# Performance work log

Hardware: AMD Instinct MI355X
Metric: run time of the kernel (lower is better)

The kernel has to match this reference:

```python
import jax, jax.numpy as jnp
import numpy as np

N = 50000          # num_entities
R = 16             # num_relations
D = 128            # embedding_dim
B = 4              # num_blocks
d = D // B         # block size (32)
E = 800000         # num edges


def setup_inputs() -> dict:
    key = jax.random.key(0)
    ks = jax.random.split(key, 9)
    s = 1.0 / np.sqrt(D)
    return {
        "edge_index": jax.random.randint(ks[0], (2, E), 0, N),
        "edge_type": jax.random.randint(ks[1], (E,), 0, R),
        "node_emb": jax.random.normal(ks[2], (N, D), jnp.float32) * s,
        "W1": jax.random.normal(ks[3], (R, B, d, d), jnp.float32) * s,
        "root1": jax.random.normal(ks[4], (D, D), jnp.float32) * s,
        "bias1": jax.random.normal(ks[5], (D,), jnp.float32) * 0.01,
        "W2": jax.random.normal(ks[6], (R, B, d, d), jnp.float32) * s,
        "root2": jax.random.normal(ks[7], (D, D), jnp.float32) * s,
        "bias2": jax.random.normal(ks[8], (D,), jnp.float32) * 0.01,
    }


def _rgcn_conv(x, src, dst, et, W, root, bias):
    # x: [N, D]; W: [R, B, d, d] block-diagonal per-relation weights.
    n = x.shape[0]
    # Transform every node under every relation (cheaper than gathering
    # per-edge weight blocks): [R, N, B, d] -> [R, N, D]
    allR = jnp.einsum('nbi,rbio->rnbo', x.reshape(n, B, d), W).reshape(R, n, D)
    msg = allR[et, src]                                   # [E, D] gather
    # Per-relation mean normalization 1/c_{i,r} (PyG RGCNConv aggr='mean'
    # applied per relation): count edges per (dst, relation) pair.
    seg = dst * R + et
    cnt = jax.ops.segment_sum(jnp.ones_like(et, x.dtype), seg, num_segments=n * R)
    norm = 1.0 / jnp.maximum(cnt[seg], 1.0)               # [E]
    agg = jax.ops.segment_sum(msg * norm[:, None], dst, num_segments=n)
    return agg + x @ root + bias


def reference(edge_index, edge_type, node_emb, W1, root1, bias1, W2, root2, bias2):
    src, dst = edge_index[0], edge_index[1]
    h = _rgcn_conv(node_emb, src, dst, edge_type, W1, root1, bias1)
    h = jax.nn.relu(h)  # dropout is identity in eval mode
    return _rgcn_conv(h, src, dst, edge_type, W2, root2, bias2)
```

## Files before the change

### kernel.cpp

```cpp
#include <hip/hip_runtime.h>
#include <hip/hip_bf16.h>

#define N_NODES 50000
#define N_REL   16
#define DIM     128
#define NBLK    4
#define BS      32
#define N_EDGES 800000
#define NSEG    (N_NODES * N_REL)
#define SCAN_BLK 1024
#define N_SCAN_BLKS ((NSEG + SCAN_BLK - 1) / SCAN_BLK)
#define NWT     (N_NODES / 16)

typedef __attribute__((ext_vector_type(8))) short s8v;
typedef __attribute__((ext_vector_type(8))) unsigned short u8v;
typedef __attribute__((ext_vector_type(4))) float f4v;

__device__ __forceinline__ float bf2f(unsigned short u) {
    return __uint_as_float(((unsigned int)u) << 16);
}
__device__ __forceinline__ unsigned short f2bfbits(float f) {
    unsigned int u = __float_as_uint(f);
    return (unsigned short)((u + 0x7fffu + ((u >> 16) & 1u)) >> 16);
}

__global__ __launch_bounds__(256) void count_kernel(const int* __restrict__ src,
                                                    const int* __restrict__ dst,
                                                    const int* __restrict__ et,
                                                    int* __restrict__ cnt,
                                                    int* __restrict__ used, int E) {
    int e = blockIdx.x * 256 + threadIdx.x;
    if (e < E) {
        int r = et[e];
        atomicAdd(&cnt[dst[e] * N_REL + r], 1);
        used[r * N_NODES + src[e]] = 1;
    }
}

__global__ __launch_bounds__(256) void scan1j_kernel(const int* __restrict__ cnt,
                                                     const int* __restrict__ used,
                                                     int* __restrict__ off,
                                                     int* __restrict__ cmap,
                                                     int2* __restrict__ bsum, int M) {
    const int t = threadIdx.x;
    const int base = blockIdx.x * SCAN_BLK + t * 4;
    int c[4], u[4];
#pragma unroll
    for (int i = 0; i < 4; ++i) {
        int idx = base + i;
        c[i] = (idx < M) ? cnt[idx] : 0;
        u[i] = (idx < M) ? used[idx] : 0;
    }
    int cs = c[0] + c[1] + c[2] + c[3];
    int us = u[0] + u[1] + u[2] + u[3];
    const int lane = t & 63, wid = t >> 6;
    int cinc = cs, uinc = us;
    for (int d = 1; d < 64; d <<= 1) {
        int a = __shfl_up(cinc, d, 64);
        int b = __shfl_up(uinc, d, 64);
        if (lane >= d) { cinc += a; uinc += b; }
    }
    __shared__ int cw[5], uw[5];
    if (lane == 63) { cw[wid] = cinc; uw[wid] = uinc; }
    __syncthreads();
    if (t == 0) {
        int a = 0, b = 0;
        for (int w = 0; w < 4; ++w) {
            int x = cw[w]; cw[w] = a; a += x;
            int y = uw[w]; uw[w] = b; b += y;
        }
        cw[4] = a; uw[4] = b;
    }
    __syncthreads();
    int cex = cinc - cs + cw[wid];
    int uex = uinc - us + uw[wid];
#pragma unroll
    for (int i = 0; i < 4; ++i) {
        int idx = base + i;
        if (idx < M) { off[idx] = cex; cmap[idx] = uex; }
        cex += c[i]; uex += u[i];
    }
    if (t == 0) bsum[blockIdx.x] = make_int2(cw[4], uw[4]);
}

__global__ __launch_bounds__(1024) void scan2j_kernel(int2* __restrict__ bsum, int nb) {
    const int t = threadIdx.x;
    int2 s = (t < nb) ? bsum[t] : make_int2(0, 0);
    const int lane = t & 63, wid = t >> 6;
    int ci = s.x, ui = s.y;
    for (int d = 1; d < 64; d <<= 1) {
        int a = __shfl_up(ci, d, 64);
        int b = __shfl_up(ui, d, 64);
        if (lane >= d) { ci += a; ui += b; }
    }
    __shared__ int cw[16], uw[16];
    if (lane == 63) { cw[wid] = ci; uw[wid] = ui; }
    __syncthreads();
    if (t == 0) {
        int a = 0, b = 0;
        for (int w = 0; w < 16; ++w) {
            int x = cw[w]; cw[w] = a; a += x;
            int y = uw[w]; uw[w] = b; b += y;
        }
    }
    __syncthreads();
    if (t < nb) bsum[t] = make_int2(ci - s.x + cw[wid], ui - s.y + uw[wid]);
}

__global__ __launch_bounds__(256) void scatter_fast_kernel(const int* __restrict__ src,
                                                           const int* __restrict__ dst,
                                                           const int* __restrict__ et,
                                                           int* __restrict__ off,
                                                           const int* __restrict__ cnt,
                                                           const int* __restrict__ cmap,
                                                           const int2* __restrict__ bsum,
                                                           int2* __restrict__ evec, int E) {
    int e = blockIdx.x * 256 + threadIdx.x;
    if (e < E) {
        int r = et[e];
        int seg = dst[e] * N_REL + r;
        int pos = atomicAdd(&off[seg], 1) + bsum[seg >> 10].x;
        float inv = 1.0f / (float)cnt[seg];
        int grow = r * N_NODES + src[e];
        int g = cmap[grow] + bsum[grow >> 10].y;
        evec[pos] = make_int2(g, __float_as_int(inv));
    }
}

__global__ __launch_bounds__(256) void scan1_kernel(const int* __restrict__ in,
                                                    int* __restrict__ out,
                                                    int* __restrict__ bsum, int M) {
    const int t = threadIdx.x;
    const int base = blockIdx.x * SCAN_BLK + t * 4;
    int v0 = (base + 0 < M) ? in[base + 0] : 0;
    int v1 = (base + 1 < M) ? in[base + 1] : 0;
    int v2 = (base + 2 < M) ? in[base + 2] : 0;
    int v3 = (base + 3 < M) ? in[base + 3] : 0;
    const int s = v0 + v1 + v2 + v3;
    const int lane = t & 63, wid = t >> 6;
    int inc = s;
    for (int d = 1; d < 64; d <<= 1) {
        int u = __shfl_up(inc, d, 64);
        if (lane >= d) inc += u;
    }
    __shared__ int wsum[5];
    if (lane == 63) wsum[wid] = inc;
    __syncthreads();
    if (t == 0) {
        int a = 0;
        for (int w = 0; w < 4; ++w) { int u = wsum[w]; wsum[w] = a; a += u; }
        wsum[4] = a;
    }
    __syncthreads();
    const int ex = inc - s + wsum[wid];
    if (base + 0 < M) out[base + 0] = ex;
    if (base + 1 < M) out[base + 1] = ex + v0;
    if (base + 2 < M) out[base + 2] = ex + v0 + v1;
    if (base + 3 < M) out[base + 3] = ex + v0 + v1 + v2;
    if (t == 0) bsum[blockIdx.x] = wsum[4];
}

__global__ __launch_bounds__(1024) void scan2_kernel(int* __restrict__ bsum, int nb) {
    const int t = threadIdx.x;
    int s = (t < nb) ? bsum[t] : 0;
    const int lane = t & 63, wid = t >> 6;
    int inc = s;
    for (int d = 1; d < 64; d <<= 1) {
        int u = __shfl_up(inc, d, 64);
        if (lane >= d) inc += u;
    }
    __shared__ int wsum[16];
    if (lane == 63) wsum[wid] = inc;
    __syncthreads();
    if (t == 0) {
        int a = 0;
        for (int w = 0; w < 16; ++w) { int u = wsum[w]; wsum[w] = a; a += u; }
    }
    __syncthreads();
    const int ex = inc - s + wsum[wid];
    if (t < nb) bsum[t] = ex;
}

__global__ __launch_bounds__(256) void scan3_kernel(int* __restrict__ out,
                                                    const int* __restrict__ bsum, int M) {
    int i = blockIdx.x * 256 + threadIdx.x;
    if (i < M) out[i] += bsum[i / SCAN_BLK];
}

__global__ __launch_bounds__(256) void scatter_old_kernel(const int* __restrict__ src,
                                                          const int* __restrict__ dst,
                                                          const int* __restrict__ et,
                                                          int* __restrict__ off,
                                                          int* __restrict__ srcs, int E) {
    int e = blockIdx.x * 256 + threadIdx.x;
    if (e < E) {
        int seg = dst[e] * N_REL + et[e];
        int pos = atomicAdd(&off[seg], 1);
        srcs[pos] = src[e];
    }
}

__global__ __launch_bounds__(256) void prep_kernel(const float* __restrict__ W1,
                                                   const float* __restrict__ W2,
                                                   const float* __restrict__ r1,
                                                   const float* __restrict__ r2,
                                                   ushort* __restrict__ WB1,
                                                   ushort* __restrict__ WB2,
                                                   ushort* __restrict__ RB1,
                                                   ushort* __restrict__ RB2) {
    int t = blockIdx.x * 256 + threadIdx.x;
    if (t < 262144) {
        const float* W = (t < 131072) ? W1 : W2;
        ushort* WB     = (t < 131072) ? WB1 : WB2;
        int idx = t & 131071;
        int i  = idx & 7;
        int lm = (idx >> 3) & 15;
        int kg = (idx >> 7) & 3;
        int mt = (idx >> 9) & 1;
        int b  = (idx >> 10) & 3;
        int r  = idx >> 12;
        WB[idx] = f2bfbits(W[((size_t)(r * 4 + b) * 32 + kg * 8 + i) * 32 + mt * 16 + lm]);
    } else if (t < 294912) {
        int u = t - 262144;
        const float* R = (u < 16384) ? r1 : r2;
        ushort* RB     = (u < 16384) ? RB1 : RB2;
        int idx = u & 16383;
        int i  = idx & 7;
        int lm = (idx >> 3) & 15;
        int kg = (idx >> 7) & 3;
        int kc = (idx >> 9) & 3;
        int mt = (idx >> 11) & 7;
        RB[idx] = f2bfbits(R[(size_t)(kc * 32 + kg * 8 + i) * DIM + mt * 16 + lm]);
    }
}

template<bool IN_BF16, bool OUT_BF16, bool RELU>
__global__ __launch_bounds__(256) void fused_kernel(const void* __restrict__ xin,
                                                    const ushort* __restrict__ WB,
                                                    const ushort* __restrict__ RB,
                                                    const float* __restrict__ bias,
                                                    const int* __restrict__ used,
                                                    const int* __restrict__ cmap,
                                                    const int2* __restrict__ bsum,
                                                    char* __restrict__ tab,
                                                    float* __restrict__ scl,
                                                    void* __restrict__ outv) {
    const int wv = threadIdx.x >> 6;
    const int l  = threadIdx.x & 63;
    const int wt = blockIdx.x * 4 + wv;
    if (wt >= NWT) return;
    const int rbase = blockIdx.y * 8;
    const int lm = l & 15;
    const int kg = l >> 4;
    const int node = wt * 16 + lm;

    s8v bfr[4];
#pragma unroll
    for (int b = 0; b < 4; ++b) {
        if (IN_BF16) {
            const ushort* xp = (const ushort*)xin + (size_t)node * DIM + b * BS + kg * 8;
            u8v u = *(const u8v*)xp;
#pragma unroll
            for (int i = 0; i < 8; ++i) {
                unsigned short us = u[i];
                if (RELU) us = (us & 0x8000u) ? (unsigned short)0 : us;
                bfr[b][i] = (short)us;
            }
        } else {
            const float* xp = (const float*)xin + (size_t)node * DIM + b * BS + kg * 8;
#pragma unroll
            for (int i = 0; i < 8; ++i) {
                float v = xp[i];
                if (RELU) v = fmaxf(v, 0.f);
                bfr[b][i] = (short)f2bfbits(v);
            }
        }
    }

#pragma unroll 2
    for (int ri = 0; ri < 8; ++ri) {
        const int rr = rbase + ri;
        const int grow = rr * N_NODES + node;
        const int flag = used[grow];
        const int cid  = cmap[grow] + bsum[grow >> 10].y;
        f4v acc[4][2];
#pragma unroll
        for (int b = 0; b < 4; ++b) {
#pragma unroll
            for (int mt = 0; mt < 2; ++mt) {
                s8v afrag = *(const s8v*)&WB[((((rr * 4 + b) * 2 + mt) * 4 + kg) * 16 + lm) * 8];
                f4v z = {0.f, 0.f, 0.f, 0.f};
                acc[b][mt] = __builtin_amdgcn_mfma_f32_16x16x32_bf16(afrag, bfr[b], z, 0, 0, 0);
            }
        }
        float t8[8];
#pragma unroll
        for (int b = 0; b < 4; ++b)
#pragma unroll
            for (int mt = 0; mt < 2; ++mt)
                t8[b * 2 + mt] = fmaxf(fmaxf(fabsf(acc[b][mt][0]), fabsf(acc[b][mt][1])),
                                       fmaxf(fabsf(acc[b][mt][2]), fabsf(acc[b][mt][3])));
        float m = fmaxf(fmaxf(fmaxf(t8[0], t8[1]), fmaxf(t8[2], t8[3])),
                        fmaxf(fmaxf(t8[4], t8[5]), fmaxf(t8[6], t8[7])));
        m = fmaxf(m, __shfl_xor(m, 16, 64));
        m = fmaxf(m, __shfl_xor(m, 32, 64));
        m = fmaxf(m, 1e-30f);

        if (flag) {
            const float qs = 127.0f / m;
            unsigned int d[8];
#pragma unroll
            for (int b = 0; b < 4; ++b) {
#pragma unroll
                for (int mt = 0; mt < 2; ++mt) {
                    int q0 = __float2int_rn(acc[b][mt][0] * qs);
                    int q1 = __float2int_rn(acc[b][mt][1] * qs);
                    int q2 = __float2int_rn(acc[b][mt][2] * qs);
                    int q3 = __float2int_rn(acc[b][mt][3] * qs);
                    unsigned int t01 = __builtin_amdgcn_perm((unsigned)q1, (unsigned)q0, 0x00000400u);
                    unsigned int t23 = __builtin_amdgcn_perm((unsigned)q3, (unsigned)q2, 0x00000400u);
                    d[b * 2 + mt] = __builtin_amdgcn_perm(t23, t01, 0x05040100u);
                }
            }
            char* gp = tab + (size_t)cid * 128 + kg * 32;
            *(uint4*)gp        = make_uint4(d[0], d[1], d[2], d[3]);
            *(uint4*)(gp + 16) = make_uint4(d[4], d[5], d[6], d[7]);
            if (kg == 0) scl[cid] = m * (1.0f / 127.0f);
        }
    }

    if (blockIdx.y == 0) {
#pragma unroll 2
        for (int mt = 0; mt < 8; ++mt) {
            const int col0 = mt * 16 + kg * 4;
            f4v acc = *(const f4v*)&bias[col0];
#pragma unroll
            for (int kc = 0; kc < 4; ++kc) {
                s8v afrag = *(const s8v*)&RB[(((mt * 4 + kc) * 4 + kg) * 16 + lm) * 8];
                acc = __builtin_amdgcn_mfma_f32_16x16x32_bf16(afrag, bfr[kc], acc, 0, 0, 0);
            }
            if (OUT_BF16) {
                unsigned int p0 = (unsigned int)f2bfbits(acc[0]) |
                                  ((unsigned int)f2bfbits(acc[1]) << 16);
                unsigned int p1 = (unsigned int)f2bfbits(acc[2]) |
                                  ((unsigned int)f2bfbits(acc[3]) << 16);
                *(uint2*)((ushort*)outv + (size_t)node * DIM + col0) = make_uint2(p0, p1);
            } else {
                *(f4v*)((float*)outv + (size_t)node * DIM + col0) = acc;
            }
        }
    }
}

template<bool OUT_BF16>
__global__ __launch_bounds__(256) void agg8_kernel(const int2* __restrict__ evec,
                                                   const int* __restrict__ off,
                                                   const int2* __restrict__ bsum,
                                                   const char* __restrict__ tab,
                                                   const float* __restrict__ scl,
                                                   void* __restrict__ outv) {
    const int hw = threadIdx.x >> 5;
    const int o  = threadIdx.x & 31;
    const int v  = blockIdx.x * 8 + hw;

    const int ei = v * N_REL + N_REL - 1;
    const int end = off[ei] + bsum[ei >> 10].x;
    int start = 0;
    if (v > 0) {
        const int si = v * N_REL - 1;
        start = off[si] + bsum[si >> 10].x;
    }

    const int p = o >> 4;
    const int w = o & 15;

    float acc[8];
#pragma unroll
    for (int j = 0; j < 8; ++j) acc[j] = 0.f;

#pragma unroll 2
    for (int base = start; base < end; base += 4) {
        const int k0 = base + p;
        const int k1 = base + 2 + p;
        const int2 e0 = evec[min(k0, end - 1)];
        const int2 e1 = evec[min(k1, end - 1)];
        const int g0 = e0.x, g1 = e1.x;
        const float i0 = (k0 < end) ? __int_as_float(e0.y) : 0.f;
        const float i1 = (k1 < end) ? __int_as_float(e1.y) : 0.f;
        const uint2 q0 = *(const uint2*)(tab + (size_t)g0 * 128 + w * 8);
        const uint2 q1 = *(const uint2*)(tab + (size_t)g1 * 128 + w * 8);
        const float s0 = scl[g0] * i0;
        const float s1 = scl[g1] * i1;
#pragma unroll
        for (int j = 0; j < 4; ++j) {
            acc[j]     = fmaf((float)(int)(signed char)(q0.x >> (8 * j)), s0, acc[j]);
            acc[4 + j] = fmaf((float)(int)(signed char)(q0.y >> (8 * j)), s0, acc[4 + j]);
        }
#pragma unroll
        for (int j = 0; j < 4; ++j) {
            acc[j]     = fmaf((float)(int)(signed char)(q1.x >> (8 * j)), s1, acc[j]);
            acc[4 + j] = fmaf((float)(int)(signed char)(q1.y >> (8 * j)), s1, acc[4 + j]);
        }
    }
#pragma unroll
    for (int j = 0; j < 8; ++j)
        acc[j] += __shfl_xor(acc[j], 16, 32);

    if (o < 16) {
        const int base0 = (o & 3) * 32 + (o >> 2) * 4;
        if (OUT_BF16) {
            ushort* hp = (ushort*)outv + (size_t)v * DIM + base0;
            ushort4 a0 = *(ushort4*)hp;
            ushort4 a1 = *(ushort4*)(hp + 16);
            a0.x = f2bfbits(bf2f(a0.x) + acc[0]);
            a0.y = f2bfbits(bf2f(a0.y) + acc[1]);
            a0.z = f2bfbits(bf2f(a0.z) + acc[2]);
            a0.w = f2bfbits(bf2f(a0.w) + acc[3]);
            a1.x = f2bfbits(bf2f(a1.x) + acc[4]);
            a1.y = f2bfbits(bf2f(a1.y) + acc[5]);
            a1.z = f2bfbits(bf2f(a1.z) + acc[6]);
            a1.w = f2bfbits(bf2f(a1.w) + acc[7]);
            *(ushort4*)hp        = a0;
            *(ushort4*)(hp + 16) = a1;
        } else {
            float* op = (float*)outv + (size_t)v * DIM + base0;
            float4 r0 = *(float4*)op;
            float4 r1 = *(float4*)(op + 16);
            r0.x += acc[0]; r0.y += acc[1]; r0.z += acc[2]; r0.w += acc[3];
            r1.x += acc[4]; r1.y += acc[5]; r1.z += acc[6]; r1.w += acc[7];
            *(float4*)op        = r0;
            *(float4*)(op + 16) = r1;
        }
    }
}

template<bool RELU>
__global__ __launch_bounds__(256) void dense_old_kernel(const float* __restrict__ x,
                                                        const float* __restrict__ root,
                                                        const float* __restrict__ bias,
                                                        float* __restrict__ out) {
    const int wv = threadIdx.x >> 6;
    const int l  = threadIdx.x & 63;
    const int wt = blockIdx.x * 4 + wv;
    if (wt >= NWT) return;
    const int nbase = wt * 16;
    const int lm = l & 15;
    const int kg = l >> 4;
    const int node = nbase + lm;

    s8v bfr[4];
#pragma unroll
    for (int kc = 0; kc < 4; ++kc) {
        const float* xp = &x[(size_t)node * DIM + kc * BS + kg * 8];
#pragma unroll
        for (int i = 0; i < 8; ++i) {
            float v = xp[i];
            if (RELU) v = fmaxf(v, 0.f);
            bfr[kc][i] = (short)f2bfbits(v);
        }
    }
#pragma unroll 2
    for (int mt = 0; mt < 8; ++mt) {
        const int col0 = mt * 16 + kg * 4;
        f4v acc = *(const f4v*)&bias[col0];
#pragma unroll
        for (int kc = 0; kc < 4; ++kc) {
            const float* rp = &root[(size_t)(kc * BS + kg * 8) * DIM + mt * 16 + lm];
            s8v afrag;
#pragma unroll
            for (int i = 0; i < 8; ++i)
                afrag[i] = (short)f2bfbits(rp[i * DIM]);
            acc = __builtin_amdgcn_mfma_f32_16x16x32_bf16(afrag, bfr[kc], acc, 0, 0, 0);
        }
        *(f4v*)&out[(size_t)node * DIM + col0] = acc;
    }
}

template<bool RELU>
__global__ __launch_bounds__(256) void agg_fallback_kernel(const int* __restrict__ srcs,
                                                           const int* __restrict__ off,
                                                           const int* __restrict__ cnt,
                                                           const float* __restrict__ x,
                                                           const float* __restrict__ W,
                                                           float* __restrict__ out) {
    __shared__ float Wsh[N_REL * BS * BS];
    const int bblk = blockIdx.y;
    for (int idx = threadIdx.x * 4; idx < N_REL * BS * BS; idx += 1024) {
        int r = idx >> 10, rest = idx & 1023;
        *(float4*)&Wsh[idx] = *(const float4*)&W[(r * NBLK + bblk) * 1024 + rest];
    }
    __syncthreads();
    const int hw = threadIdx.x >> 5;
    const int o  = threadIdx.x & 31;
    const int v  = blockIdx.x * 8 + hw;
    int endv = 0, cv = 0;
    if (o < N_REL) { endv = off[v * N_REL + o]; cv = cnt[v * N_REL + o]; }
    float acc = out[v * DIM + bblk * BS + o];
    for (int r = 0; r < N_REL; ++r) {
        const int c = __shfl(cv, r, 32);
        if (c == 0) continue;
        const int end = __shfl(endv, r, 32);
        float xs = 0.f;
        for (int k = end - c; k < end; ++k) {
            const int s = srcs[k];
            float xv = x[s * DIM + bblk * BS + o];
            if (RELU) xv = fmaxf(xv, 0.f);
            xs += xv;
        }
        xs *= (1.0f / (float)c);
        const float* wr = &Wsh[r * (BS * BS)];
#pragma unroll
        for (int i = 0; i < BS; i += 2) {
            float xi0 = __shfl(xs, i, 32);
            float xi1 = __shfl(xs, i + 1, 32);
            acc = fmaf(xi0, wr[i * BS + o], acc);
            acc = fmaf(xi1, wr[(i + 1) * BS + o], acc);
        }
    }
    out[v * DIM + bblk * BS + o] = acc;
}

extern "C" void kernel_launch(void* const* d_in, const int* in_sizes, int n_in,
                              void* d_out, int out_size, void* d_ws, size_t ws_size,
                              hipStream_t stream) {
    const int*   edge_index = (const int*)d_in[0];
    const int*   src   = edge_index;
    const int*   dstv  = edge_index + N_EDGES;
    const int*   et    = (const int*)d_in[1];
    const float* x0    = (const float*)d_in[2];
    const float* W1    = (const float*)d_in[3];
    const float* root1 = (const float*)d_in[4];
    const float* bias1 = (const float*)d_in[5];
    const float* W2    = (const float*)d_in[6];
    const float* root2 = (const float*)d_in[7];
    const float* bias2 = (const float*)d_in[8];
    float* out = (float*)d_out;

    char* ws = (char*)d_ws;
    ushort* h    = (ushort*)ws;
    int*    cnt  = (int*)   (ws + 12800000);
    int*    used = (int*)   (ws + 16000000);
    int*    off  = (int*)   (ws + 19200000);
    int*    cmap = (int*)   (ws + 22400000);
    int2*   evec = (int2*)  (ws + 25600000);
    int2*   bsum = (int2*)  (ws + 32000000);
    ushort* WB1  = (ushort*)(ws + 32008192);
    ushort* WB2  = (ushort*)(ws + 32270336);
    ushort* RB1  = (ushort*)(ws + 32532480);
    ushort* RB2  = (ushort*)(ws + 32565248);
    float*  scl  = (float*) (ws + 32598016);
    char*   tab  =          (ws + 35798016);
    const size_t FAST_NEED = 138198016ull;

    const int egrid = (N_EDGES + 255) / 256;
    const int tgrid = (NWT + 3) / 4;

    if (ws_size >= FAST_NEED) {
        prep_kernel<<<1152, 256, 0, stream>>>(W1, W2, root1, root2, WB1, WB2, RB1, RB2);
        hipMemsetAsync(cnt, 0, 2 * (size_t)NSEG * sizeof(int), stream);
        count_kernel<<<egrid, 256, 0, stream>>>(src, dstv, et, cnt, used, N_EDGES);
        scan1j_kernel<<<N_SCAN_BLKS, 256, 0, stream>>>(cnt, used, off, cmap, bsum, NSEG);
        scan2j_kernel<<<1, 1024, 0, stream>>>(bsum, N_SCAN_BLKS);
        scatter_fast_kernel<<<egrid, 256, 0, stream>>>(src, dstv, et, off, cnt, cmap,
                                                       bsum, evec, N_EDGES);

        dim3 fgrid(tgrid, 2);
        const int ngrid = N_NODES / 8;

        fused_kernel<false, true, false><<<fgrid, 256, 0, stream>>>(
            x0, WB1, RB1, bias1, used, cmap, bsum, tab, scl, h);
        agg8_kernel<true><<<ngrid, 256, 0, stream>>>(evec, off, bsum, tab, scl, h);

        fused_kernel<true, false, true><<<fgrid, 256, 0, stream>>>(
            h, WB2, RB2, bias2, used, cmap, bsum, tab, scl, out);
        agg8_kernel<false><<<ngrid, 256, 0, stream>>>(evec, off, bsum, tab, scl, out);
    } else {
        float* hf    = (float*)d_ws;
        int*   cntf  = (int*)((char*)d_ws + 25600000);
        int*   offf  = (int*)((char*)d_ws + 28800000);
        int*   srcsf = (int*)((char*)d_ws + 32000000);
        int*   bsumf = (int*)((char*)d_ws + 35200000);
        int*   usedD = offf;

        hipMemsetAsync(cntf, 0, (size_t)NSEG * sizeof(int), stream);
        count_kernel<<<egrid, 256, 0, stream>>>(src, dstv, et, cntf, usedD, N_EDGES);
        scan1_kernel<<<N_SCAN_BLKS, 256, 0, stream>>>(cntf, offf, bsumf, NSEG);
        scan2_kernel<<<1, 1024, 0, stream>>>(bsumf, N_SCAN_BLKS);
        scan3_kernel<<<(NSEG + 255) / 256, 256, 0, stream>>>(offf, bsumf, NSEG);
        scatter_old_kernel<<<egrid, 256, 0, stream>>>(src, dstv, et, offf, srcsf, N_EDGES);

        dim3 fgrid2(N_NODES / 8, NBLK);
        dense_old_kernel<false><<<tgrid, 256, 0, stream>>>(x0, root1, bias1, hf);
        agg_fallback_kernel<false><<<fgrid2, 256, 0, stream>>>(srcsf, offf, cntf, x0, W1, hf);
        dense_old_kernel<true><<<tgrid, 256, 0, stream>>>(hf, root2, bias2, out);
        agg_fallback_kernel<true><<<fgrid2, 256, 0, stream>>>(srcsf, offf, cntf, hf, W2, out);
    }
}
```

Before: 244.6 us.

## Fuse edge scatter into first transform kernel, zero counters in prep, split root work

The per-edge CSR scatter now runs as extra blocks of the first fused transform launch, so edge placement overlaps with the relation transforms and one launch is removed. The counter memset is folded into the prep kernel as a grid-stride zero loop. The dense root/bias epilogue is split across the two relation halves instead of being done only by the y=0 half. Int8 quantisation uses a magic-number FMA in place of float-to-int conversions. The fallback count kernel no longer writes into the offset buffer. Risks are heavier kernels and scatter blocks competing for resources with the transform blocks.

```diff
diff --git a/kernel.cpp b/kernel.cpp
--- a/kernel.cpp
+++ b/kernel.cpp
@@ -11,6 +11,8 @@
 #define SCAN_BLK 1024
 #define N_SCAN_BLKS ((NSEG + SCAN_BLK - 1) / SCAN_BLK)
 #define NWT     (N_NODES / 16)
+#define NWTB    ((NWT + 3) / 4)
+#define SCATB   ((N_EDGES + 511) / 512)
 
 typedef __attribute__((ext_vector_type(8))) short s8v;
 typedef __attribute__((ext_vector_type(8))) unsigned short u8v;
@@ -22,182 +24,6 @@
 __device__ __forceinline__ unsigned short f2bfbits(float f) {
     unsigned int u = __float_as_uint(f);
     return (unsigned short)((u + 0x7fffu + ((u >> 16) & 1u)) >> 16);
-}
-
-__global__ __launch_bounds__(256) void count_kernel(const int* __restrict__ src,
-                                                    const int* __restrict__ dst,
-                                                    const int* __restrict__ et,
-                                                    int* __restrict__ cnt,
-                                                    int* __restrict__ used, int E) {
-    int e = blockIdx.x * 256 + threadIdx.x;
-    if (e < E) {
-        int r = et[e];
-        atomicAdd(&cnt[dst[e] * N_REL + r], 1);
-        used[r * N_NODES + src[e]] = 1;
-    }
-}
-
-__global__ __launch_bounds__(256) void scan1j_kernel(const int* __restrict__ cnt,
-                                                     const int* __restrict__ used,
-                                                     int* __restrict__ off,
-                                                     int* __restrict__ cmap,
-                                                     int2* __restrict__ bsum, int M) {
-    const int t = threadIdx.x;
-    const int base = blockIdx.x * SCAN_BLK + t * 4;
-    int c[4], u[4];
-#pragma unroll
-    for (int i = 0; i < 4; ++i) {
-        int idx = base + i;
-        c[i] = (idx < M) ? cnt[idx] : 0;
-        u[i] = (idx < M) ? used[idx] : 0;
-    }
-    int cs = c[0] + c[1] + c[2] + c[3];
-    int us = u[0] + u[1] + u[2] + u[3];
-    const int lane = t & 63, wid = t >> 6;
-    int cinc = cs, uinc = us;
-    for (int d = 1; d < 64; d <<= 1) {
-        int a = __shfl_up(cinc, d, 64);
-        int b = __shfl_up(uinc, d, 64);
-        if (lane >= d) { cinc += a; uinc += b; }
-    }
-    __shared__ int cw[5], uw[5];
-    if (lane == 63) { cw[wid] = cinc; uw[wid] = uinc; }
-    __syncthreads();
-    if (t == 0) {
-        int a = 0, b = 0;
-        for (int w = 0; w < 4; ++w) {
-            int x = cw[w]; cw[w] = a; a += x;
-            int y = uw[w]; uw[w] = b; b += y;
-        }
-        cw[4] = a; uw[4] = b;
-    }
-    __syncthreads();
-    int cex = cinc - cs + cw[wid];
-    int uex = uinc - us + uw[wid];
-#pragma unroll
-    for (int i = 0; i < 4; ++i) {
-        int idx = base + i;
-        if (idx < M) { off[idx] = cex; cmap[idx] = uex; }
-        cex += c[i]; uex += u[i];
-    }
-    if (t == 0) bsum[blockIdx.x] = make_int2(cw[4], uw[4]);
-}
-
-__global__ __launch_bounds__(1024) void scan2j_kernel(int2* __restrict__ bsum, int nb) {
-    const int t = threadIdx.x;
-    int2 s = (t < nb) ? bsum[t] : make_int2(0, 0);
-    const int lane = t & 63, wid = t >> 6;
-    int ci = s.x, ui = s.y;
-    for (int d = 1; d < 64; d <<= 1) {
-        int a = __shfl_up(ci, d, 64);
-        int b = __shfl_up(ui, d, 64);
-        if (lane >= d) { ci += a; ui += b; }
-    }
-    __shared__ int cw[16], uw[16];
-    if (lane == 63) { cw[wid] = ci; uw[wid] = ui; }
-    __syncthreads();
-    if (t == 0) {
-        int a = 0, b = 0;
-        for (int w = 0; w < 16; ++w) {
-            int x = cw[w]; cw[w] = a; a += x;
-            int y = uw[w]; uw[w] = b; b += y;
-        }
-    }
-    __syncthreads();
-    if (t < nb) bsum[t] = make_int2(ci - s.x + cw[wid], ui - s.y + uw[wid]);
-}
-
-__global__ __launch_bounds__(256) void scatter_fast_kernel(const int* __restrict__ src,
-                                                           const int* __restrict__ dst,
-                                                           const int* __restrict__ et,
-                                                           int* __restrict__ off,
-                                                           const int* __restrict__ cnt,
-                                                           const int* __restrict__ cmap,
-                                                           const int2* __restrict__ bsum,
-                                                           int2* __restrict__ evec, int E) {
-    int e = blockIdx.x * 256 + threadIdx.x;
-    if (e < E) {
-        int r = et[e];
-        int seg = dst[e] * N_REL + r;
-        int pos = atomicAdd(&off[seg], 1) + bsum[seg >> 10].x;
-        float inv = 1.0f / (float)cnt[seg];
-        int grow = r * N_NODES + src[e];
-        int g = cmap[grow] + bsum[grow >> 10].y;
-        evec[pos] = make_int2(g, __float_as_int(inv));
-    }
-}
-
-__global__ __launch_bounds__(256) void scan1_kernel(const int* __restrict__ in,
-                                                    int* __restrict__ out,
-                                                    int* __restrict__ bsum, int M) {
-    const int t = threadIdx.x;
-    const int base = blockIdx.x * SCAN_BLK + t * 4;
-    int v0 = (base + 0 < M) ? in[base + 0] : 0;
-    int v1 = (base + 1 < M) ? in[base + 1] : 0;
-    int v2 = (base + 2 < M) ? in[base + 2] : 0;
-    int v3 = (base + 3 < M) ? in[base + 3] : 0;
-    const int s = v0 + v1 + v2 + v3;
-    const int lane = t & 63, wid = t >> 6;
-    int inc = s;
-    for (int d = 1; d < 64; d <<= 1) {
-        int u = __shfl_up(inc, d, 64);
-        if (lane >= d) inc += u;
-    }
-    __shared__ int wsum[5];
-    if (lane == 63) wsum[wid] = inc;
-    __syncthreads();
-    if (t == 0) {
-        int a = 0;
-        for (int w = 0; w < 4; ++w) { int u = wsum[w]; wsum[w] = a; a += u; }
-        wsum[4] = a;
-    }
-    __syncthreads();
-    const int ex = inc - s + wsum[wid];
-    if (base + 0 < M) out[base + 0] = ex;
-    if (base + 1 < M) out[base + 1] = ex + v0;
-    if (base + 2 < M) out[base + 2] = ex + v0 + v1;
-    if (base + 3 < M) out[base + 3] = ex + v0 + v1 + v2;
-    if (t == 0) bsum[blockIdx.x] = wsum[4];
-}
-
-__global__ __launch_bounds__(1024) void scan2_kernel(int* __restrict__ bsum, int nb) {
-    const int t = threadIdx.x;
-    int s = (t < nb) ? bsum[t] : 0;
-    const int lane = t & 63, wid = t >> 6;
-    int inc = s;
-    for (int d = 1; d < 64; d <<= 1) {
-        int u = __shfl_up(inc, d, 64);
-        if (lane >= d) inc += u;
-    }
-    __shared__ int wsum[16];
-    if (lane == 63) wsum[wid] = inc;
-    __syncthreads();
-    if (t == 0) {
-        int a = 0;
-        for (int w = 0; w < 16; ++w) { int u = wsum[w]; wsum[w] = a; a += u; }
-    }
-    __syncthreads();
-    const int ex = inc - s + wsum[wid];
-    if (t < nb) bsum[t] = ex;
-}
-
-__global__ __launch_bounds__(256) void scan3_kernel(int* __restrict__ out,
-                                                    const int* __restrict__ bsum, int M) {
-    int i = blockIdx.x * 256 + threadIdx.x;
-    if (i < M) out[i] += bsum[i / SCAN_BLK];
-}
-
-__global__ __launch_bounds__(256) void scatter_old_kernel(const int* __restrict__ src,
-                                                          const int* __restrict__ dst,
-                                                          const int* __restrict__ et,
-                                                          int* __restrict__ off,
-                                                          int* __restrict__ srcs, int E) {
-    int e = blockIdx.x * 256 + threadIdx.x;
-    if (e < E) {
-        int seg = dst[e] * N_REL + et[e];
-        int pos = atomicAdd(&off[seg], 1);
-        srcs[pos] = src[e];
-    }
 }
 
 __global__ __launch_bounds__(256) void prep_kernel(const float* __restrict__ W1,
@@ -207,8 +33,12 @@
                                                    ushort* __restrict__ WB1,
                                                    ushort* __restrict__ WB2,
                                                    ushort* __restrict__ RB1,
-                                                   ushort* __restrict__ RB2) {
+                                                   ushort* __restrict__ RB2,
+                                                   uint4* __restrict__ zero_base) {
     int t = blockIdx.x * 256 + threadIdx.x;
+    for (int i = t; i < (2 * NSEG) / 4; i += 1152 * 256)
+        zero_base[i] = make_uint4(0u, 0u, 0u, 0u);
+
     if (t < 262144) {
         const float* W = (t < 131072) ? W1 : W2;
         ushort* WB     = (t < 131072) ? WB1 : WB2;
@@ -234,7 +64,163 @@
     }
 }
 
-template<bool IN_BF16, bool OUT_BF16, bool RELU>
+__global__ __launch_bounds__(256) void count_kernel(const int* __restrict__ src,
+                                                    const int* __restrict__ dst,
+                                                    const int* __restrict__ et,
+                                                    int* __restrict__ cnt,
+                                                    int* __restrict__ used, int E) {
+    int e = blockIdx.x * 256 + threadIdx.x;
+    if (e < E) {
+        int r = et[e];
+        atomicAdd(&cnt[dst[e] * N_REL + r], 1);
+        used[r * N_NODES + src[e]] = 1;
+    }
+}
+
+__global__ __launch_bounds__(256) void scan1j_kernel(const int* __restrict__ cnt,
+                                                     const int* __restrict__ used,
+                                                     int* __restrict__ off,
+                                                     int* __restrict__ cmap,
+                                                     int2* __restrict__ bsum, int M) {
+    const int t = threadIdx.x;
+    const int base = blockIdx.x * SCAN_BLK + t * 4;
+    int c[4], u[4];
+#pragma unroll
+    for (int i = 0; i < 4; ++i) {
+        int idx = base + i;
+        c[i] = (idx < M) ? cnt[idx] : 0;
+        u[i] = (idx < M) ? used[idx] : 0;
+    }
+    int cs = c[0] + c[1] + c[2] + c[3];
+    int us = u[0] + u[1] + u[2] + u[3];
+    const int lane = t & 63, wid = t >> 6;
+    int cinc = cs, uinc = us;
+    for (int d = 1; d < 64; d <<= 1) {
+        int a = __shfl_up(cinc, d, 64);
+        int b = __shfl_up(uinc, d, 64);
+        if (lane >= d) { cinc += a; uinc += b; }
+    }
+    __shared__ int cw[5], uw[5];
+    if (lane == 63) { cw[wid] = cinc; uw[wid] = uinc; }
+    __syncthreads();
+    if (t == 0) {
+        int a = 0, b = 0;
+        for (int w = 0; w < 4; ++w) {
+            int x = cw[w]; cw[w] = a; a += x;
+            int y = uw[w]; uw[w] = b; b += y;
+        }
+        cw[4] = a; uw[4] = b;
+    }
+    __syncthreads();
+    int cex = cinc - cs + cw[wid];
+    int uex = uinc - us + uw[wid];
+#pragma unroll
+    for (int i = 0; i < 4; ++i) {
+        int idx = base + i;
+        if (idx < M) { off[idx] = cex; cmap[idx] = uex; }
+        cex += c[i]; uex += u[i];
+    }
+    if (t == 0) bsum[blockIdx.x] = make_int2(cw[4], uw[4]);
+}
+
+__global__ __launch_bounds__(1024) void scan2j_kernel(int2* __restrict__ bsum, int nb) {
+    const int t = threadIdx.x;
+    int2 s = (t < nb) ? bsum[t] : make_int2(0, 0);
+    const int lane = t & 63, wid = t >> 6;
+    int ci = s.x, ui = s.y;
+    for (int d = 1; d < 64; d <<= 1) {
+        int a = __shfl_up(ci, d, 64);
+        int b = __shfl_up(ui, d, 64);
+        if (lane >= d) { ci += a; ui += b; }
+    }
+    __shared__ int cw[16], uw[16];
+    if (lane == 63) { cw[wid] = ci; uw[wid] = ui; }
+    __syncthreads();
+    if (t == 0) {
+        int a = 0, b = 0;
+        for (int w = 0; w < 16; ++w) {
+            int x = cw[w]; cw[w] = a; a += x;
+            int y = uw[w]; uw[w] = b; b += y;
+        }
+    }
+    __syncthreads();
+    if (t < nb) bsum[t] = make_int2(ci - s.x + cw[wid], ui - s.y + uw[wid]);
+}
+
+__global__ __launch_bounds__(256) void scan1_kernel(const int* __restrict__ in,
+                                                    int* __restrict__ out,
+                                                    int* __restrict__ bsum, int M) {
+    const int t = threadIdx.x;
+    const int base = blockIdx.x * SCAN_BLK + t * 4;
+    int v0 = (base + 0 < M) ? in[base + 0] : 0;
+    int v1 = (base + 1 < M) ? in[base + 1] : 0;
+    int v2 = (base + 2 < M) ? in[base + 2] : 0;
+    int v3 = (base + 3 < M) ? in[base + 3] : 0;
+    const int s = v0 + v1 + v2 + v3;
+    const int lane = t & 63, wid = t >> 6;
+    int inc = s;
+    for (int d = 1; d < 64; d <<= 1) {
+        int u = __shfl_up(inc, d, 64);
+        if (lane >= d) inc += u;
+    }
+    __shared__ int wsum[5];
+    if (lane == 63) wsum[wid] = inc;
+    __syncthreads();
+    if (t == 0) {
+        int a = 0;
+        for (int w = 0; w < 4; ++w) { int u = wsum[w]; wsum[w] = a; a += u; }
+        wsum[4] = a;
+    }
+    __syncthreads();
+    const int ex = inc - s + wsum[wid];
+    if (base + 0 < M) out[base + 0] = ex;
+    if (base + 1 < M) out[base + 1] = ex + v0;
+    if (base + 2 < M) out[base + 2] = ex + v0 + v1;
+    if (base + 3 < M) out[base + 3] = ex + v0 + v1 + v2;
+    if (t == 0) bsum[blockIdx.x] = wsum[4];
+}
+
+__global__ __launch_bounds__(1024) void scan2_kernel(int* __restrict__ bsum, int nb) {
+    const int t = threadIdx.x;
+    int s = (t < nb) ? bsum[t] : 0;
+    const int lane = t & 63, wid = t >> 6;
+    int inc = s;
+    for (int d = 1; d < 64; d <<= 1) {
+        int u = __shfl_up(inc, d, 64);
+        if (lane >= d) inc += u;
+    }
+    __shared__ int wsum[16];
+    if (lane == 63) wsum[wid] = inc;
+    __syncthreads();
+    if (t == 0) {
+        int a = 0;
+        for (int w = 0; w < 16; ++w) { int u = wsum[w]; wsum[w] = a; a += u; }
+    }
+    __syncthreads();
+    const int ex = inc - s + wsum[wid];
+    if (t < nb) bsum[t] = ex;
+}
+
+__global__ __launch_bounds__(256) void scan3_kernel(int* __restrict__ out,
+                                                    const int* __restrict__ bsum, int M) {
+    int i = blockIdx.x * 256 + threadIdx.x;
+    if (i < M) out[i] += bsum[i / SCAN_BLK];
+}
+
+__global__ __launch_bounds__(256) void scatter_old_kernel(const int* __restrict__ src,
+                                                          const int* __restrict__ dst,
+                                                          const int* __restrict__ et,
+                                                          int* __restrict__ off,
+                                                          int* __restrict__ srcs, int E) {
+    int e = blockIdx.x * 256 + threadIdx.x;
+    if (e < E) {
+        int seg = dst[e] * N_REL + et[e];
+        int pos = atomicAdd(&off[seg], 1);
+        srcs[pos] = src[e];
+    }
+}
+
+template<bool IN_BF16, bool OUT_BF16, bool RELU, bool WITH_SCATTER>
 __global__ __launch_bounds__(256) void fused_kernel(const void* __restrict__ xin,
                                                     const ushort* __restrict__ WB,
                                                     const ushort* __restrict__ RB,
@@ -244,12 +230,39 @@
                                                     const int2* __restrict__ bsum,
                                                     char* __restrict__ tab,
                                                     float* __restrict__ scl,
-                                                    void* __restrict__ outv) {
+                                                    void* __restrict__ outv,
+                                                    const int* __restrict__ src,
+                                                    const int* __restrict__ dstv,
+                                                    const int* __restrict__ et,
+                                                    int* __restrict__ off,
+                                                    const int* __restrict__ cnt,
+                                                    int2* __restrict__ evec) {
+    const int bid = blockIdx.x;
+    if (WITH_SCATTER && bid >= 2 * NWTB) {
+        const int e0 = (bid - 2 * NWTB) * 512 + threadIdx.x;
+#pragma unroll
+        for (int q = 0; q < 2; ++q) {
+            const int e = e0 + q * 256;
+            if (e < N_EDGES) {
+                int r = et[e];
+                int seg = dstv[e] * N_REL + r;
+                int pos = atomicAdd(&off[seg], 1) + bsum[seg >> 10].x;
+                float inv = 1.0f / (float)cnt[seg];
+                int grow = r * N_NODES + src[e];
+                int g = cmap[grow] + bsum[grow >> 10].y;
+                evec[pos] = make_int2(g, __float_as_int(inv));
+            }
+        }
+        return;
+    }
+
+    const int ybit = (bid >= NWTB) ? 1 : 0;
+    const int xb   = bid - ybit * NWTB;
     const int wv = threadIdx.x >> 6;
     const int l  = threadIdx.x & 63;
-    const int wt = blockIdx.x * 4 + wv;
+    const int wt = xb * 4 + wv;
     if (wt >= NWT) return;
-    const int rbase = blockIdx.y * 8;
+    const int rbase = ybit * 8;
     const int lm = l & 15;
     const int kg = l >> 4;
     const int node = wt * 16 + lm;
@@ -277,6 +290,7 @@
         }
     }
 
+    const float MAGIC = 12582912.0f;
 #pragma unroll 2
     for (int ri = 0; ri < 8; ++ri) {
         const int rr = rbase + ri;
@@ -313,12 +327,12 @@
             for (int b = 0; b < 4; ++b) {
 #pragma unroll
                 for (int mt = 0; mt < 2; ++mt) {
-                    int q0 = __float2int_rn(acc[b][mt][0] * qs);
-                    int q1 = __float2int_rn(acc[b][mt][1] * qs);
-                    int q2 = __float2int_rn(acc[b][mt][2] * qs);
-                    int q3 = __float2int_rn(acc[b][mt][3] * qs);
-                    unsigned int t01 = __builtin_amdgcn_perm((unsigned)q1, (unsigned)q0, 0x00000400u);
-                    unsigned int t23 = __builtin_amdgcn_perm((unsigned)q3, (unsigned)q2, 0x00000400u);
+                    unsigned f0 = __float_as_uint(fmaf(acc[b][mt][0], qs, MAGIC));
+                    unsigned f1 = __float_as_uint(fmaf(acc[b][mt][1], qs, MAGIC));
+                    unsigned f2 = __float_as_uint(fmaf(acc[b][mt][2], qs, MAGIC));
+                    unsigned f3 = __float_as_uint(fmaf(acc[b][mt][3], qs, MAGIC));
+                    unsigned t01 = __builtin_amdgcn_perm(f1, f0, 0x00000400u);
+                    unsigned t23 = __builtin_amdgcn_perm(f3, f2, 0x00000400u);
                     d[b * 2 + mt] = __builtin_amdgcn_perm(t23, t01, 0x05040100u);
                 }
             }
@@ -329,9 +343,10 @@
         }
     }
 
-    if (blockIdx.y == 0) {
+    {
+        const int mt0 = ybit * 4;
 #pragma unroll 2
-        for (int mt = 0; mt < 8; ++mt) {
+        for (int mt = mt0; mt < mt0 + 4; ++mt) {
             const int col0 = mt * 16 + kg * 4;
             f4v acc = *(const f4v*)&bias[col0];
 #pragma unroll
@@ -434,6 +449,13 @@
     }
 }
 
+__global__ __launch_bounds__(256) void count_fb_kernel(const int* __restrict__ dst,
+                                                       const int* __restrict__ et,
+                                                       int* __restrict__ cnt, int E) {
+    int e = blockIdx.x * 256 + threadIdx.x;
+    if (e < E) atomicAdd(&cnt[dst[e] * N_REL + et[e]], 1);
+}
+
 template<bool RELU>
 __global__ __launch_bounds__(256) void dense_old_kernel(const float* __restrict__ x,
                                                         const float* __restrict__ root,
@@ -553,26 +575,24 @@
     const size_t FAST_NEED = 138198016ull;
 
     const int egrid = (N_EDGES + 255) / 256;
-    const int tgrid = (NWT + 3) / 4;
 
     if (ws_size >= FAST_NEED) {
-        prep_kernel<<<1152, 256, 0, stream>>>(W1, W2, root1, root2, WB1, WB2, RB1, RB2);
-        hipMemsetAsync(cnt, 0, 2 * (size_t)NSEG * sizeof(int), stream);
+        prep_kernel<<<1152, 256, 0, stream>>>(W1, W2, root1, root2, WB1, WB2,
+                                              RB1, RB2, (uint4*)cnt);
         count_kernel<<<egrid, 256, 0, stream>>>(src, dstv, et, cnt, used, N_EDGES);
         scan1j_kernel<<<N_SCAN_BLKS, 256, 0, stream>>>(cnt, used, off, cmap, bsum, NSEG);
         scan2j_kernel<<<1, 1024, 0, stream>>>(bsum, N_SCAN_BLKS);
-        scatter_fast_kernel<<<egrid, 256, 0, stream>>>(src, dstv, et, off, cnt, cmap,
-                                                       bsum, evec, N_EDGES);
-
-        dim3 fgrid(tgrid, 2);
+
         const int ngrid = N_NODES / 8;
 
-        fused_kernel<false, true, false><<<fgrid, 256, 0, stream>>>(
-            x0, WB1, RB1, bias1, used, cmap, bsum, tab, scl, h);
+        fused_kernel<false, true, false, true><<<2 * NWTB + SCATB, 256, 0, stream>>>(
+            x0, WB1, RB1, bias1, used, cmap, bsum, tab, scl, h,
+            src, dstv, et, off, cnt, evec);
         agg8_kernel<true><<<ngrid, 256, 0, stream>>>(evec, off, bsum, tab, scl, h);
 
-        fused_kernel<true, false, true><<<fgrid, 256, 0, stream>>>(
-            h, WB2, RB2, bias2, used, cmap, bsum, tab, scl, out);
+        fused_kernel<true, false, true, false><<<2 * NWTB, 256, 0, stream>>>(
+            h, WB2, RB2, bias2, used, cmap, bsum, tab, scl, out,
+            src, dstv, et, off, cnt, evec);
         agg8_kernel<false><<<ngrid, 256, 0, stream>>>(evec, off, bsum, tab, scl, out);
     } else {
         float* hf    = (float*)d_ws;
@@ -580,19 +600,18 @@
         int*   offf  = (int*)((char*)d_ws + 28800000);
         int*   srcsf = (int*)((char*)d_ws + 32000000);
         int*   bsumf = (int*)((char*)d_ws + 35200000);
-        int*   usedD = offf;
 
         hipMemsetAsync(cntf, 0, (size_t)NSEG * sizeof(int), stream);
-        count_kernel<<<egrid, 256, 0, stream>>>(src, dstv, et, cntf, usedD, N_EDGES);
+        count_fb_kernel<<<egrid, 256, 0, stream>>>(dstv, et, cntf, N_EDGES);
         scan1_kernel<<<N_SCAN_BLKS, 256, 0, stream>>>(cntf, offf, bsumf, NSEG);
         scan2_kernel<<<1, 1024, 0, stream>>>(bsumf, N_SCAN_BLKS);
         scan3_kernel<<<(NSEG + 255) / 256, 256, 0, stream>>>(offf, bsumf, NSEG);
         scatter_old_kernel<<<egrid, 256, 0, stream>>>(src, dstv, et, offf, srcsf, N_EDGES);
 
         dim3 fgrid2(N_NODES / 8, NBLK);
-        dense_old_kernel<false><<<tgrid, 256, 0, stream>>>(x0, root1, bias1, hf);
+        dense_old_kernel<false><<<NWTB, 256, 0, stream>>>(x0, root1, bias1, hf);
         agg_fallback_kernel<false><<<fgrid2, 256, 0, stream>>>(srcsf, offf, cntf, x0, W1, hf);
-        dense_old_kernel<true><<<tgrid, 256, 0, stream>>>(hf, root2, bias2, out);
+        dense_old_kernel<true><<<NWTB, 256, 0, stream>>>(hf, root2, bias2, out);
         agg_fallback_kernel<true><<<fgrid2, 256, 0, stream>>>(srcsf, offf, cntf, hf, W2, out);
     }
 }
```

New measurement: 229.7 us. 6.1% less time.
